# Kernel optimization log

Hardware: AMD Instinct MI355X
Metric: run time of the kernel (lower is better)

Reference implementation:

```python
import jax, jax.numpy as jnp
import numpy as np

B, C, H, W = 2, 3, 96, 96
OC = 2  # conv output channels
EPS = 1e-5

def setup_inputs() -> dict:
    key = jax.random.key(0)
    k1, k2, k3, k4 = jax.random.split(key, 4)
    return {
        "X_tnext": jax.random.normal(k1, (B, C, H, W), dtype=jnp.float32),
        "X_hat_tnext": jax.random.normal(k2, (B, C, H, W), dtype=jnp.float32),
        "conv_w": jax.random.normal(k3, (OC, C, 3, 3), dtype=jnp.float32) * 0.1,
        "conv_b": jax.random.normal(k4, (OC,), dtype=jnp.float32) * 0.1,
        "gamma": jnp.ones((OC,), dtype=jnp.float32),
        "beta": jnp.zeros((OC,), dtype=jnp.float32),
    }

def reference(X_tnext, X_hat_tnext, conv_w, conv_b, gamma, beta):
    b, c, h, w = X_tnext.shape
    n = h * w
    q = X_tnext.reshape(b, c, n)
    k = X_hat_tnext.reshape(b, c, n)
    # corr4D: [b, n, n] = q^T k / sqrt(c)  (materialized O(N^2) volume, as in source)
    corr = jnp.einsum('bcn,bcm->bnm', q, k) / jnp.sqrt(jnp.asarray(c, jnp.float32))
    # weighted aggregation: corr @ X_tnext (broadcast over channels)
    agg = jnp.einsum('bnm,bcm->bcn', corr, q).reshape(b, c, h, w)
    # Conv2d(3->2, k=3, s=1, p=1)
    y = jax.lax.conv_general_dilated(
        agg, conv_w, window_strides=(1, 1), padding='SAME',
        dimension_numbers=('NCHW', 'OIHW', 'NCHW'))
    y = y + conv_b[None, :, None, None]
    # BatchNorm2d (training-mode batch statistics, biased var, eps=1e-5)
    mean = jnp.mean(y, axis=(0, 2, 3), keepdims=True)
    var = jnp.var(y, axis=(0, 2, 3), keepdims=True)
    y = (y - mean) * jax.lax.rsqrt(var + EPS)
    y = y * gamma[None, :, None, None] + beta[None, :, None, None]
    # LeakyReLU(0.1)
    return jnp.where(y >= 0, y, 0.1 * y)
```

## Files before the change

kernel.cpp:

```cpp
#include <hip/hip_runtime.h>
#include <math.h>

namespace {
constexpr int kB = 2, kC = 3, kOC = 2, kH = 96, kW = 96;
constexpr int kN      = kH * kW;
constexpr int kChunks = kN / 256;
constexpr int kBlocks = kB * kChunks;
constexpr float kEps   = 1e-5f;
constexpr float kScale = 0.57735026918962576f;
constexpr int WS_P = 0;
constexpr int WS_Y = 512;
}

__global__ __launch_bounds__(256) void kA_conv(const float* __restrict__ X,
                                               const float* __restrict__ Xh,
                                               const float* __restrict__ cw,
                                               const float* __restrict__ cb,
                                               float* __restrict__ ws) {
    const int tid = threadIdx.x;
    const int blk = blockIdx.x;
    const int b   = blk / kChunks;
    const int pix = (blk % kChunks) * 256 + tid;
    const int h = pix / kW, w = pix % kW;

    const float*  qb  = X  + (size_t)b * kC * kN;
    const float4* qb4 = (const float4*)qb;
    const float4* kb4 = (const float4*)(Xh + (size_t)b * kC * kN);
    float m[9] = {0,0,0,0,0,0,0,0,0};
    for (int n = tid; n < kN / 4; n += 256) {
        const float4 q0 = qb4[n], q1 = qb4[kN/4 + n], q2 = qb4[2*kN/4 + n];
        const float4 k0 = kb4[n], k1 = kb4[kN/4 + n], k2 = kb4[2*kN/4 + n];
        m[0] += k0.x*q0.x + k0.y*q0.y + k0.z*q0.z + k0.w*q0.w;
        m[1] += k0.x*q1.x + k0.y*q1.y + k0.z*q1.z + k0.w*q1.w;
        m[2] += k0.x*q2.x + k0.y*q2.y + k0.z*q2.z + k0.w*q2.w;
        m[3] += k1.x*q0.x + k1.y*q0.y + k1.z*q0.z + k1.w*q0.w;
        m[4] += k1.x*q1.x + k1.y*q1.y + k1.z*q1.z + k1.w*q1.w;
        m[5] += k1.x*q2.x + k1.y*q2.y + k1.z*q2.z + k1.w*q2.w;
        m[6] += k2.x*q0.x + k2.y*q0.y + k2.z*q0.z + k2.w*q0.w;
        m[7] += k2.x*q1.x + k2.y*q1.y + k2.z*q1.z + k2.w*q1.w;
        m[8] += k2.x*q2.x + k2.y*q2.y + k2.z*q2.z + k2.w*q2.w;
    }
    #pragma unroll
    for (int off = 32; off > 0; off >>= 1) {
        #pragma unroll
        for (int j = 0; j < 9; ++j) m[j] += __shfl_down(m[j], off);
    }
    __shared__ float sMw[4][9];
    __shared__ float sM[9];
    __shared__ float sE[2][3][9];
    if ((tid & 63) == 0) {
        #pragma unroll
        for (int j = 0; j < 9; ++j) sMw[tid >> 6][j] = m[j];
    }
    __syncthreads();
    if (tid < 9) sM[tid] = sMw[0][tid] + sMw[1][tid] + sMw[2][tid] + sMw[3][tid];
    __syncthreads();
    if (tid < 54) {
        const int oc = tid / 27, r = tid % 27, cp = r / 9, nb = r % 9;
        sE[oc][cp][nb] = kScale * (cw[oc * 27 +      nb] * sM[cp * 3 + 0] +
                                   cw[oc * 27 +  9 + nb] * sM[cp * 3 + 1] +
                                   cw[oc * 27 + 18 + nb] * sM[cp * 3 + 2]);
    }
    __syncthreads();

    float acc0 = cb[0], acc1 = cb[1];
    #pragma unroll
    for (int dh = 0; dh < 3; ++dh) {
        const int hh = h + dh - 1;
        if (hh < 0 || hh >= kH) continue;
        #pragma unroll
        for (int dw = 0; dw < 3; ++dw) {
            const int ww = w + dw - 1;
            if (ww < 0 || ww >= kW) continue;
            const int p = hh * kW + ww, nb = dh * 3 + dw;
            const float q0 = qb[p], q1 = qb[kN + p], q2 = qb[2 * kN + p];
            acc0 += q0 * sE[0][0][nb] + q1 * sE[0][1][nb] + q2 * sE[0][2][nb];
            acc1 += q0 * sE[1][0][nb] + q1 * sE[1][1][nb] + q2 * sE[1][2][nb];
        }
    }
    ((float2*)(ws + WS_Y))[(size_t)b * kN + pix] = make_float2(acc0, acc1);

    float v0 = acc0, v1 = acc0 * acc0, v2 = acc1, v3 = acc1 * acc1;
    #pragma unroll
    for (int off = 32; off > 0; off >>= 1) {
        v0 += __shfl_down(v0, off); v1 += __shfl_down(v1, off);
        v2 += __shfl_down(v2, off); v3 += __shfl_down(v3, off);
    }
    __shared__ float sP[4][4];
    if ((tid & 63) == 0) {
        const int wv = tid >> 6;
        sP[wv][0] = v0; sP[wv][1] = v1; sP[wv][2] = v2; sP[wv][3] = v3;
    }
    __syncthreads();
    if (tid < 4)
        ws[WS_P + blk * 4 + tid] = sP[0][tid] + sP[1][tid] + sP[2][tid] + sP[3][tid];
}

__global__ __launch_bounds__(256) void kB_bn(const float* __restrict__ ws,
                                             const float* __restrict__ gamma,
                                             const float* __restrict__ beta,
                                             float* __restrict__ out) {
    const int tid = threadIdx.x;
    const int blk = blockIdx.x;
    const int b   = blk / kChunks;
    const int pix = (blk % kChunks) * 256 + tid;

    __shared__ float4 sR[128];
    if (tid < 128) {
        float4 p = make_float4(0.f, 0.f, 0.f, 0.f);
        if (tid < kBlocks) p = ((const float4*)(ws + WS_P))[tid];
        sR[tid] = p;
    }
    __syncthreads();
    for (int s = 64; s > 0; s >>= 1) {
        if (tid < s) {
            float4 a = sR[tid], c = sR[tid + s];
            sR[tid] = make_float4(a.x + c.x, a.y + c.y, a.z + c.z, a.w + c.w);
        }
        __syncthreads();
    }
    const float4 tot = sR[0];
    const float inv   = 1.f / (float)(kB * kN);
    const float mean0 = tot.x * inv, mean1 = tot.z * inv;
    const float g0 = gamma[0] * rsqrtf(tot.y * inv - mean0 * mean0 + kEps);
    const float g1 = gamma[1] * rsqrtf(tot.w * inv - mean1 * mean1 + kEps);
    const float b0 = beta[0], b1 = beta[1];

    const float2 y2 = ((const float2*)(ws + WS_Y))[(size_t)b * kN + pix];
    float y0 = (y2.x - mean0) * g0 + b0;
    float y1 = (y2.y - mean1) * g1 + b1;
    out[(size_t)(b * kOC + 0) * kN + pix] = (y0 >= 0.f) ? y0 : 0.1f * y0;
    out[(size_t)(b * kOC + 1) * kN + pix] = (y1 >= 0.f) ? y1 : 0.1f * y1;
}

extern "C" void kernel_launch(void* const* d_in, const int* in_sizes, int n_in,
                              void* d_out, int out_size, void* d_ws, size_t ws_size,
                              hipStream_t stream) {
    const float* X      = (const float*)d_in[0];
    const float* Xhat   = (const float*)d_in[1];
    const float* conv_w = (const float*)d_in[2];
    const float* conv_b = (const float*)d_in[3];
    const float* gamma  = (const float*)d_in[4];
    const float* beta   = (const float*)d_in[5];
    float* ws = (float*)d_ws;

    kA_conv<<<kBlocks, 256, 0, stream>>>(X, Xhat, conv_w, conv_b, ws);
    kB_bn  <<<kBlocks, 256, 0, stream>>>(ws, gamma, beta, (float*)d_out);
}
```

Measured before the change: 73.17 us.

## Fuse conv and batchnorm kernels with a grid-wide atomic barrier

Merges the conv/statistics kernel and the batchnorm/activation kernel into one launch. An atomic counter barrier across all 72 blocks waits until every block has written its partial sums, so each block keeps its conv results in registers instead of writing them to and reading them from workspace. It also fully unrolls the 3x3 Gram loop and issues the stencil neighbour loads early, before the reductions, so their latency overlaps. It adds a memset launch to reset the counter, and it depends on all blocks being resident at once, which holds at this grid size.

```diff
diff --git a/kernel.cpp b/kernel.cpp
--- a/kernel.cpp
+++ b/kernel.cpp
@@ -8,15 +8,18 @@
 constexpr int kBlocks = kB * kChunks;
 constexpr float kEps   = 1e-5f;
 constexpr float kScale = 0.57735026918962576f;
-constexpr int WS_P = 0;
-constexpr int WS_Y = 512;
+constexpr int WS_P     = 0;
+constexpr int WS_CTR_B = 1280;
 }
 
-__global__ __launch_bounds__(256) void kA_conv(const float* __restrict__ X,
+__global__ __launch_bounds__(256) void k_fused(const float* __restrict__ X,
                                                const float* __restrict__ Xh,
                                                const float* __restrict__ cw,
                                                const float* __restrict__ cb,
-                                               float* __restrict__ ws) {
+                                               const float* __restrict__ gamma,
+                                               const float* __restrict__ beta,
+                                               float* __restrict__ ws,
+                                               float* __restrict__ out) {
     const int tid = threadIdx.x;
     const int blk = blockIdx.x;
     const int b   = blk / kChunks;
@@ -26,8 +29,11 @@
     const float*  qb  = X  + (size_t)b * kC * kN;
     const float4* qb4 = (const float4*)qb;
     const float4* kb4 = (const float4*)(Xh + (size_t)b * kC * kN);
+
     float m[9] = {0,0,0,0,0,0,0,0,0};
-    for (int n = tid; n < kN / 4; n += 256) {
+    #pragma unroll
+    for (int it = 0; it < 9; ++it) {
+        const int n = it * 256 + tid;
         const float4 q0 = qb4[n], q1 = qb4[kN/4 + n], q2 = qb4[2*kN/4 + n];
         const float4 k0 = kb4[n], k1 = kb4[kN/4 + n], k2 = kb4[2*kN/4 + n];
         m[0] += k0.x*q0.x + k0.y*q0.y + k0.z*q0.z + k0.w*q0.w;
@@ -40,6 +46,23 @@
         m[7] += k2.x*q1.x + k2.y*q1.y + k2.z*q1.z + k2.w*q1.w;
         m[8] += k2.x*q2.x + k2.y*q2.y + k2.z*q2.z + k2.w*q2.w;
     }
+
+    float qt0[9], qt1[9], qt2[9];
+    #pragma unroll
+    for (int dh = 0; dh < 3; ++dh) {
+        #pragma unroll
+        for (int dw = 0; dw < 3; ++dw) {
+            const int hh = h + dh - 1, ww = w + dw - 1;
+            const bool ok = (hh >= 0) && (hh < kH) && (ww >= 0) && (ww < kW);
+            const int p = ok ? hh * kW + ww : pix;
+            const int t = dh * 3 + dw;
+            const float f0 = qb[p], f1 = qb[kN + p], f2 = qb[2 * kN + p];
+            qt0[t] = ok ? f0 : 0.f;
+            qt1[t] = ok ? f1 : 0.f;
+            qt2[t] = ok ? f2 : 0.f;
+        }
+    }
+
     #pragma unroll
     for (int off = 32; off > 0; off >>= 1) {
         #pragma unroll
@@ -65,20 +88,10 @@
 
     float acc0 = cb[0], acc1 = cb[1];
     #pragma unroll
-    for (int dh = 0; dh < 3; ++dh) {
-        const int hh = h + dh - 1;
-        if (hh < 0 || hh >= kH) continue;
-        #pragma unroll
-        for (int dw = 0; dw < 3; ++dw) {
-            const int ww = w + dw - 1;
-            if (ww < 0 || ww >= kW) continue;
-            const int p = hh * kW + ww, nb = dh * 3 + dw;
-            const float q0 = qb[p], q1 = qb[kN + p], q2 = qb[2 * kN + p];
-            acc0 += q0 * sE[0][0][nb] + q1 * sE[0][1][nb] + q2 * sE[0][2][nb];
-            acc1 += q0 * sE[1][0][nb] + q1 * sE[1][1][nb] + q2 * sE[1][2][nb];
-        }
+    for (int t = 0; t < 9; ++t) {
+        acc0 += qt0[t] * sE[0][0][t] + qt1[t] * sE[0][1][t] + qt2[t] * sE[0][2][t];
+        acc1 += qt0[t] * sE[1][0][t] + qt1[t] * sE[1][1][t] + qt2[t] * sE[1][2][t];
     }
-    ((float2*)(ws + WS_Y))[(size_t)b * kN + pix] = make_float2(acc0, acc1);
 
     float v0 = acc0, v1 = acc0 * acc0, v2 = acc1, v3 = acc1 * acc1;
     #pragma unroll
@@ -94,41 +107,38 @@
     __syncthreads();
     if (tid < 4)
         ws[WS_P + blk * 4 + tid] = sP[0][tid] + sP[1][tid] + sP[2][tid] + sP[3][tid];
-}
 
-__global__ __launch_bounds__(256) void kB_bn(const float* __restrict__ ws,
-                                             const float* __restrict__ gamma,
-                                             const float* __restrict__ beta,
-                                             float* __restrict__ out) {
-    const int tid = threadIdx.x;
-    const int blk = blockIdx.x;
-    const int b   = blk / kChunks;
-    const int pix = (blk % kChunks) * 256 + tid;
-
-    __shared__ float4 sR[128];
-    if (tid < 128) {
-        float4 p = make_float4(0.f, 0.f, 0.f, 0.f);
-        if (tid < kBlocks) p = ((const float4*)(ws + WS_P))[tid];
-        sR[tid] = p;
+    __syncthreads();
+    unsigned int* ctr = (unsigned int*)((char*)ws + WS_CTR_B);
+    if (tid == 0) {
+        __threadfence();
+        __hip_atomic_fetch_add(ctr, 1u, __ATOMIC_ACQ_REL, __HIP_MEMORY_SCOPE_AGENT);
+        while (__hip_atomic_load(ctr, __ATOMIC_ACQUIRE, __HIP_MEMORY_SCOPE_AGENT) < (unsigned)kBlocks)
+            __builtin_amdgcn_s_sleep(1);
     }
     __syncthreads();
-    for (int s = 64; s > 0; s >>= 1) {
-        if (tid < s) {
-            float4 a = sR[tid], c = sR[tid + s];
-            sR[tid] = make_float4(a.x + c.x, a.y + c.y, a.z + c.z, a.w + c.w);
-        }
-        __syncthreads();
+    __threadfence();
+
+    const int lane = tid & 63;
+    const float4* P4 = (const float4*)(ws + WS_P);
+    float4 s = P4[lane];
+    if (lane < kBlocks - 64) {
+        const float4 e = P4[64 + lane];
+        s.x += e.x; s.y += e.y; s.z += e.z; s.w += e.w;
     }
-    const float4 tot = sR[0];
+    #pragma unroll
+    for (int off = 32; off > 0; off >>= 1) {
+        s.x += __shfl_xor(s.x, off);
+        s.y += __shfl_xor(s.y, off);
+        s.z += __shfl_xor(s.z, off);
+        s.w += __shfl_xor(s.w, off);
+    }
     const float inv   = 1.f / (float)(kB * kN);
-    const float mean0 = tot.x * inv, mean1 = tot.z * inv;
-    const float g0 = gamma[0] * rsqrtf(tot.y * inv - mean0 * mean0 + kEps);
-    const float g1 = gamma[1] * rsqrtf(tot.w * inv - mean1 * mean1 + kEps);
-    const float b0 = beta[0], b1 = beta[1];
-
-    const float2 y2 = ((const float2*)(ws + WS_Y))[(size_t)b * kN + pix];
-    float y0 = (y2.x - mean0) * g0 + b0;
-    float y1 = (y2.y - mean1) * g1 + b1;
+    const float mean0 = s.x * inv, mean1 = s.z * inv;
+    const float g0 = gamma[0] * rsqrtf(s.y * inv - mean0 * mean0 + kEps);
+    const float g1 = gamma[1] * rsqrtf(s.w * inv - mean1 * mean1 + kEps);
+    const float y0 = (acc0 - mean0) * g0 + beta[0];
+    const float y1 = (acc1 - mean1) * g1 + beta[1];
     out[(size_t)(b * kOC + 0) * kN + pix] = (y0 >= 0.f) ? y0 : 0.1f * y0;
     out[(size_t)(b * kOC + 1) * kN + pix] = (y1 >= 0.f) ? y1 : 0.1f * y1;
 }
@@ -144,6 +154,7 @@
     const float* beta   = (const float*)d_in[5];
     float* ws = (float*)d_ws;
 
-    kA_conv<<<kBlocks, 256, 0, stream>>>(X, Xhat, conv_w, conv_b, ws);
-    kB_bn  <<<kBlocks, 256, 0, stream>>>(ws, gamma, beta, (float*)d_out);
+    hipMemsetAsync((char*)d_ws + WS_CTR_B, 0, 4, stream);
+    k_fused<<<kBlocks, 256, 0, stream>>>(X, Xhat, conv_w, conv_b, gamma, beta,
+                                         ws, (float*)d_out);
 }
```

New measurement: 78.20 us. +6.9%, slower.
